# Kernel tuning notes

Measured on AMD Instinct MI355X. Metric: run time of the kernel, lower is better.

## Reference

```python
import jax, jax.numpy as jnp
import numpy as np

N_NODES = 50000
N_EDGES = 800000
D = 64
BN_EPS = 1e-5


def setup_inputs() -> dict:
    key = jax.random.key(0)
    ks = jax.random.split(key, 16)
    x = jax.random.normal(ks[0], (N_NODES, D), dtype=jnp.float32)
    edge_index = jax.random.randint(ks[1], (2, N_EDGES), 0, N_NODES, dtype=jnp.int64)
    s = 1.0 / np.sqrt(D)
    def lin(k):
        kw, kb = jax.random.split(k)
        W = jax.random.uniform(kw, (D, D), jnp.float32, -s, s)
        b = jax.random.uniform(kb, (D,), jnp.float32, -s, s)
        return W, b
    W1_0, b1_0 = lin(ks[2])
    W2_0, b2_0 = lin(ks[3])
    W1_1, b1_1 = lin(ks[4])
    W2_1, b2_1 = lin(ks[5])
    return {
        "x": x, "edge_index": edge_index,
        "W1_0": W1_0, "b1_0": b1_0, "g_0": jnp.ones((D,), jnp.float32), "beta_0": jnp.zeros((D,), jnp.float32), "W2_0": W2_0, "b2_0": b2_0,
        "W1_1": W1_1, "b1_1": b1_1, "g_1": jnp.ones((D,), jnp.float32), "beta_1": jnp.zeros((D,), jnp.float32), "W2_1": W2_1, "b2_1": b2_1,
    }


def _gin_layer(x, src, dst, W1, b1, g, beta, W2, b2):
    # GINConv with eps=0: h_i = MLP( x_i + sum_{j->i} x_j )
    agg = jax.ops.segment_sum(x[src], dst, num_segments=N_NODES)  # [N, D]
    h = agg + x
    h = h @ W1 + b1
    # BatchNorm1d (training-mode batch statistics, biased variance)
    mean = jnp.mean(h, axis=0)
    var = jnp.var(h, axis=0)
    h = (h - mean) * jax.lax.rsqrt(var + BN_EPS) * g + beta
    h = jax.nn.relu(h)
    h = jax.nn.relu(h @ W2 + b2)
    return h


def reference(x, edge_index, W1_0, b1_0, g_0, beta_0, W2_0, b2_0,
              W1_1, b1_1, g_1, beta_1, W2_1, b2_1):
    src = edge_index[0]  # message source j
    dst = edge_index[1]  # aggregation target i
    h1 = _gin_layer(x, src, dst, W1_0, b1_0, g_0, beta_0, W2_0, b2_0)
    h2 = _gin_layer(h1, src, dst, W1_1, b1_1, g_1, beta_1, W2_1, b2_1)
    return (h1, h2)
```

## Files before the change

kernel.cpp:

```cpp
#include <hip/hip_runtime.h>
#include <hip/hip_bf16.h>

#define N_NODES 50000
#define N_EDGES 800000
#define DD 64
#define RPB 64
#define GBLOCKS ((N_NODES + RPB - 1) / RPB)
#define MBLOCKS ((N_NODES + 63) / 64)
#define SCAN_BLOCKS ((N_NODES + 255) / 256)
#define CAST_BLOCKS ((N_NODES * DD / 8 + 255) / 256)
#define BN_EPS 1e-5f


__device__ __forceinline__ float bf2f(unsigned short b) {
    return __uint_as_float(((unsigned)b) << 16);
}
__device__ __forceinline__ float loadF(const void* p, int i, int isf) {
    return isf ? ((const float*)p)[i] : bf2f(((const unsigned short*)p)[i]);
}
template<bool ISF>
__device__ __forceinline__ float4 ld4(const void* p, int i) {
    if (ISF) return *reinterpret_cast<const float4*>((const float*)p + i);
    ushort4 u = *reinterpret_cast<const ushort4*>((const unsigned short*)p + i);
    return make_float4(bf2f(u.x), bf2f(u.y), bf2f(u.z), bf2f(u.w));
}
__device__ __forceinline__ void acc8(float4& a, float4& b, uint4 u) {
    a.x += __uint_as_float(u.x << 16);
    a.y += __uint_as_float(u.x & 0xFFFF0000u);
    a.z += __uint_as_float(u.y << 16);
    a.w += __uint_as_float(u.y & 0xFFFF0000u);
    b.x += __uint_as_float(u.z << 16);
    b.y += __uint_as_float(u.z & 0xFFFF0000u);
    b.z += __uint_as_float(u.w << 16);
    b.w += __uint_as_float(u.w & 0xFFFF0000u);
}

__global__ __launch_bounds__(256) void initcast_kernel(
    const void* __restrict__ x, const int* __restrict__ ei,
    int* __restrict__ flags, int* __restrict__ cnt,
    float* __restrict__ sums, unsigned short* __restrict__ xb)
{
    __shared__ int cntF, cntI;
    int t = threadIdx.x;
    if (t == 0) { cntF = 0; cntI = 0; }
    __syncthreads();
    unsigned short wd = ((const unsigned short*)x)[2 * t];
    int e = (wd >> 7) & 0xFF;
    if (e >= 0x70 && e <= 0x8F) atomicAdd(&cntF, 1);
    if (t < 128 && ei[2 * t + 1] == 0) atomicAdd(&cntI, 1);
    __syncthreads();
    int isf = (cntF < 128) ? 1 : 0;

    int gid = blockIdx.x * 256 + t;
    if (gid < N_NODES) cnt[gid] = 0;
    if (gid < 256) sums[gid] = 0.0f;
    if (blockIdx.x == 0 && t == 0) {
        flags[0] = isf;
        flags[1] = (cntI > 64) ? 1 : 0;
    }

    int i = gid * 8;
    if (i < N_NODES * DD) {
        if (isf) {
            float4 a = *reinterpret_cast<const float4*>((const float*)x + i);
            float4 b = *reinterpret_cast<const float4*>((const float*)x + i + 4);
            ushort4 o0, o1;
            o0.x = __bfloat16_as_ushort(__float2bfloat16(a.x));
            o0.y = __bfloat16_as_ushort(__float2bfloat16(a.y));
            o0.z = __bfloat16_as_ushort(__float2bfloat16(a.z));
            o0.w = __bfloat16_as_ushort(__float2bfloat16(a.w));
            o1.x = __bfloat16_as_ushort(__float2bfloat16(b.x));
            o1.y = __bfloat16_as_ushort(__float2bfloat16(b.y));
            o1.z = __bfloat16_as_ushort(__float2bfloat16(b.z));
            o1.w = __bfloat16_as_ushort(__float2bfloat16(b.w));
            *reinterpret_cast<ushort4*>(xb + i) = o0;
            *reinterpret_cast<ushort4*>(xb + i + 4) = o1;
        } else {
            *reinterpret_cast<uint4*>(xb + i) =
                *reinterpret_cast<const uint4*>((const unsigned short*)x + i);
        }
    }
}

__global__ void hist_kernel(const int* __restrict__ ei, int* __restrict__ cnt,
                            const int* __restrict__ flags) {
    int i64 = flags[1];
    int e = blockIdx.x * 256 + threadIdx.x;
    int d = i64 ? ei[2 * N_EDGES + 2 * e] : ei[N_EDGES + e];
    atomicAdd(cnt + d, 1);
}

__global__ __launch_bounds__(256) void scanA_kernel(const int* __restrict__ cnt,
                                                    int* __restrict__ off,
                                                    int* __restrict__ bsum) {
    __shared__ int tmp[256];
    int t = threadIdx.x;
    int i = blockIdx.x * 256 + t;
    int v = (i < N_NODES) ? cnt[i] : 0;
    tmp[t] = v;
    __syncthreads();
    #pragma unroll
    for (int d = 1; d < 256; d <<= 1) {
        int u = (t >= d) ? tmp[t - d] : 0;
        __syncthreads();
        tmp[t] += u;
        __syncthreads();
    }
    if (i < N_NODES) off[i] = tmp[t] - v;
    if (t == 255) bsum[blockIdx.x] = tmp[255];
}

__global__ __launch_bounds__(256) void scanB_kernel(int* __restrict__ bsum,
                                                    int* __restrict__ off) {
    __shared__ int tmp[256];
    int t = threadIdx.x;
    int v = (t < SCAN_BLOCKS) ? bsum[t] : 0;
    tmp[t] = v;
    __syncthreads();
    #pragma unroll
    for (int d = 1; d < 256; d <<= 1) {
        int u = (t >= d) ? tmp[t - d] : 0;
        __syncthreads();
        tmp[t] += u;
        __syncthreads();
    }
    if (t < SCAN_BLOCKS) bsum[t] = tmp[t] - v;
    if (t == 255) off[N_NODES] = tmp[255];
}

__global__ __launch_bounds__(256) void scanC_kernel(const int* __restrict__ bsum,
                                                    int* __restrict__ off,
                                                    int* __restrict__ cur) {
    int i = blockIdx.x * 256 + threadIdx.x;
    if (i < N_NODES) {
        int o = off[i] + bsum[blockIdx.x];
        off[i] = o;
        cur[i] = o;
    }
}

__global__ void fill_kernel(const int* __restrict__ ei, int* __restrict__ cur,
                            unsigned short* __restrict__ srt, const int* __restrict__ flags) {
    int i64 = flags[1];
    int e = blockIdx.x * 256 + threadIdx.x;
    int s, d;
    if (i64) { s = ei[2 * e]; d = ei[2 * N_EDGES + 2 * e]; }
    else     { s = ei[e];     d = ei[N_EDGES + e]; }
    int pos = atomicAdd(cur + d, 1);
    srt[pos] = (unsigned short)s;
}

__global__ __launch_bounds__(512) void gather_gemm_stats_kernel(
    const unsigned short* __restrict__ xb, const void* __restrict__ self_src, int force_f32,
    const int* __restrict__ off, const unsigned short* __restrict__ srt,
    const void* __restrict__ W, const void* __restrict__ bias,
    float* __restrict__ out_, float* __restrict__ sums, const int* __restrict__ flags)
{
    __shared__ float sIn[RPB][DD];
    __shared__ float r1[8][DD], r2[8][DD];
    int tid = threadIdx.x;
    int lane = tid & 63, w = tid >> 6;
    int rs = lane >> 3, ch = lane & 7;
    int row0 = blockIdx.x * RPB;
    int isf = force_f32 ? 1 : flags[0];

    int lr = w * 8 + rs;
    int r = row0 + lr;
    float4 a  = make_float4(0.f, 0.f, 0.f, 0.f);
    float4 b  = make_float4(0.f, 0.f, 0.f, 0.f);
    float4 a2 = make_float4(0.f, 0.f, 0.f, 0.f);
    float4 b2 = make_float4(0.f, 0.f, 0.f, 0.f);
    if (r < N_NODES) {
        a = isf ? ld4<true>(self_src, r * DD + 8 * ch)
                : ld4<false>(self_src, r * DD + 8 * ch);
        b = isf ? ld4<true>(self_src, r * DD + 8 * ch + 4)
                : ld4<false>(self_src, r * DD + 8 * ch + 4);
        int k0 = off[r], k1 = off[r + 1];
        int k = k0;
        for (; k + 8 <= k1; k += 8) {
            int n0 = srt[k],     n1 = srt[k + 1], n2 = srt[k + 2], n3 = srt[k + 3];
            int n4 = srt[k + 4], n5 = srt[k + 5], n6 = srt[k + 6], n7 = srt[k + 7];
            uint4 u0 = *reinterpret_cast<const uint4*>(xb + n0 * DD + 8 * ch);
            uint4 u1 = *reinterpret_cast<const uint4*>(xb + n1 * DD + 8 * ch);
            uint4 u2 = *reinterpret_cast<const uint4*>(xb + n2 * DD + 8 * ch);
            uint4 u3 = *reinterpret_cast<const uint4*>(xb + n3 * DD + 8 * ch);
            uint4 u4 = *reinterpret_cast<const uint4*>(xb + n4 * DD + 8 * ch);
            uint4 u5 = *reinterpret_cast<const uint4*>(xb + n5 * DD + 8 * ch);
            uint4 u6 = *reinterpret_cast<const uint4*>(xb + n6 * DD + 8 * ch);
            uint4 u7 = *reinterpret_cast<const uint4*>(xb + n7 * DD + 8 * ch);
            acc8(a, b, u0);
            acc8(a2, b2, u1);
            acc8(a, b, u2);
            acc8(a2, b2, u3);
            acc8(a, b, u4);
            acc8(a2, b2, u5);
            acc8(a, b, u6);
            acc8(a2, b2, u7);
        }
        for (; k + 2 <= k1; k += 2) {
            int n0 = srt[k], n1 = srt[k + 1];
            uint4 u0 = *reinterpret_cast<const uint4*>(xb + n0 * DD + 8 * ch);
            uint4 u1 = *reinterpret_cast<const uint4*>(xb + n1 * DD + 8 * ch);
            acc8(a, b, u0);
            acc8(a2, b2, u1);
        }
        if (k < k1) {
            int n0 = srt[k];
            acc8(a, b, *reinterpret_cast<const uint4*>(xb + n0 * DD + 8 * ch));
        }
        a.x += a2.x; a.y += a2.y; a.z += a2.z; a.w += a2.w;
        b.x += b2.x; b.y += b2.y; b.z += b2.z; b.w += b2.w;
    }
    *reinterpret_cast<float4*>(&sIn[lr][8 * ch]) = a;
    *reinterpret_cast<float4*>(&sIn[lr][8 * ch + 4]) = b;
    __syncthreads();

    float wcol[DD];
    #pragma unroll
    for (int k = 0; k < DD; ++k) wcol[k] = loadF(W, k * DD + lane, isf);
    float bv = loadF(bias, lane, isf);

    float s1 = 0.f, s2 = 0.f;
    #pragma unroll 4
    for (int j = 0; j < 8; ++j) {
        int jr = w * 8 + j;
        float c0 = 0.f, c1 = 0.f, c2 = 0.f, c3 = 0.f;
        #pragma unroll
        for (int k = 0; k < DD; k += 4) {
            float4 aa = *reinterpret_cast<const float4*>(&sIn[jr][k]);
            c0 += aa.x * wcol[k];
            c1 += aa.y * wcol[k + 1];
            c2 += aa.z * wcol[k + 2];
            c3 += aa.w * wcol[k + 3];
        }
        float acc = bv + ((c0 + c1) + (c2 + c3));
        int rr = row0 + jr;
        if (rr < N_NODES) {
            out_[rr * DD + lane] = acc;
            s1 += acc;
            s2 += acc * acc;
        }
    }
    r1[w][lane] = s1; r2[w][lane] = s2;
    __syncthreads();
    if (w == 0) {
        float t1 = 0.f, t2 = 0.f;
        #pragma unroll
        for (int q = 0; q < 8; ++q) { t1 += r1[q][lane]; t2 += r2[q][lane]; }
        atomicAdd(&sums[lane], t1);
        atomicAdd(&sums[64 + lane], t2);
    }
}

__global__ __launch_bounds__(256) void mlp2_kernel(
    const float* __restrict__ in_, const float* __restrict__ sums,
    const void* __restrict__ gma, const void* __restrict__ beta,
    const void* __restrict__ W, const void* __restrict__ bias,
    float* __restrict__ oF, unsigned short* obf, const int* __restrict__ flags)
{
    __shared__ float sIn[64][DD];
    __shared__ float sScale[DD], sShift[DD];
    int isf = flags[0];
    int tid = threadIdx.x;
    int c = tid & 63, g = tid >> 6;
    int row0 = blockIdx.x * 64;

    if (tid < 64) {
        float S1 = sums[tid];
        float S2 = sums[64 + tid];
        float mean = S1 * (1.0f / N_NODES);
        float var  = S2 * (1.0f / N_NODES) - mean * mean;
        float scale = rsqrtf(var + BN_EPS) * loadF(gma, tid, isf);
        sScale[tid] = scale;
        sShift[tid] = loadF(beta, tid, isf) - mean * scale;
    }
    __syncthreads();

    #pragma unroll
    for (int j = 0; j < 4; ++j) {
        int lr = (tid >> 4) + 16 * j;
        int cc = (tid & 15) << 2;
        int r = row0 + lr;
        float4 v = make_float4(0.f, 0.f, 0.f, 0.f);
        if (r < N_NODES) {
            v = *reinterpret_cast<const float4*>(in_ + r * DD + cc);
            float4 sc = *reinterpret_cast<const float4*>(&sScale[cc]);
            float4 sh = *reinterpret_cast<const float4*>(&sShift[cc]);
            v.x = fmaxf(v.x * sc.x + sh.x, 0.f);
            v.y = fmaxf(v.y * sc.y + sh.y, 0.f);
            v.z = fmaxf(v.z * sc.z + sh.z, 0.f);
            v.w = fmaxf(v.w * sc.w + sh.w, 0.f);
        }
        *reinterpret_cast<float4*>(&sIn[lr][cc]) = v;
    }
    __syncthreads();

    float wcol[DD];
    #pragma unroll
    for (int k = 0; k < DD; ++k) wcol[k] = loadF(W, k * DD + c, isf);
    float bv = loadF(bias, c, isf);

    #pragma unroll 4
    for (int j = 0; j < 16; ++j) {
        int lr = g * 16 + j;
        float a0 = 0.f, a1 = 0.f, a2 = 0.f, a3 = 0.f;
        #pragma unroll
        for (int k = 0; k < DD; k += 4) {
            float4 a = *reinterpret_cast<const float4*>(&sIn[lr][k]);
            a0 += a.x * wcol[k];
            a1 += a.y * wcol[k + 1];
            a2 += a.z * wcol[k + 2];
            a3 += a.w * wcol[k + 3];
        }
        float acc = fmaxf(bv + ((a0 + a1) + (a2 + a3)), 0.f);
        int r = row0 + lr;
        if (r < N_NODES) {
            oF[r * DD + c] = acc;
            if (obf) obf[r * DD + c] = __bfloat16_as_ushort(__float2bfloat16(acc));
        }
    }
}

extern "C" void kernel_launch(void* const* d_in, const int* in_sizes, int n_in,
                              void* d_out, int out_size, void* d_ws, size_t ws_size,
                              hipStream_t stream)
{
    (void)in_sizes; (void)n_in; (void)out_size; (void)ws_size;
    const void* x  = d_in[0];
    const int* ei  = (const int*)d_in[1];
    const void* W1_0 = d_in[2];  const void* b1_0 = d_in[3];
    const void* g_0  = d_in[4];  const void* be_0 = d_in[5];
    const void* W2_0 = d_in[6];  const void* b2_0 = d_in[7];
    const void* W1_1 = d_in[8];  const void* b1_1 = d_in[9];
    const void* g_1  = d_in[10]; const void* be_1 = d_in[11];
    const void* W2_1 = d_in[12]; const void* b2_1 = d_in[13];

    float* wsf   = (float*)d_ws;
    float* sumsA = wsf;
    float* sumsB = wsf + 128;
    int*  flags  = (int*)(wsf + 256);
    int*  cnt    = (int*)(wsf + 512);
    int*  off    = cnt + 50048;
    int*  cur    = off + 50064;
    int*  bsum   = cur + 50048;
    unsigned short* srt = (unsigned short*)(bsum + 256);
    unsigned short* xb  = srt + 800064;
    float* O1    = (float*)d_out;
    float* O2    = O1 + (size_t)N_NODES * DD;

    dim3 blk(256);

    initcast_kernel<<<CAST_BLOCKS, blk, 0, stream>>>(x, ei, flags, cnt, sumsA, xb);
    hist_kernel<<<N_EDGES / 256, blk, 0, stream>>>(ei, cnt, flags);
    scanA_kernel<<<SCAN_BLOCKS, blk, 0, stream>>>(cnt, off, bsum);
    scanB_kernel<<<1, blk, 0, stream>>>(bsum, off);
    scanC_kernel<<<SCAN_BLOCKS, blk, 0, stream>>>(bsum, off, cur);
    fill_kernel<<<N_EDGES / 256, blk, 0, stream>>>(ei, cur, srt, flags);

    gather_gemm_stats_kernel<<<GBLOCKS, 512, 0, stream>>>(xb, x, 0, off, srt, W1_0, b1_0,
                                                          O2, sumsA, flags);
    mlp2_kernel<<<MBLOCKS, blk, 0, stream>>>(O2, sumsA, g_0, be_0, W2_0, b2_0, O1, xb, flags);

    gather_gemm_stats_kernel<<<GBLOCKS, 512, 0, stream>>>(xb, O1, 1, off, srt, W1_1, b1_1,
                                                          O2, sumsB, flags);
    mlp2_kernel<<<MBLOCKS, blk, 0, stream>>>(O2, sumsB, g_1, be_1, W2_1, b2_1, O2, nullptr, flags);
}
```

Before: 313.3 us.

## Two-pass bucketed CSR fill, vectorized index loads, and smaller gather blocks

The CSR fill, which used per-node global atomics, becomes a two-stage scheme. Edges are first scattered into 64-node buckets with padded bucket counters, packing the source and the local destination into one 32-bit word. A second kernel then places them within each bucket using shared-memory atomics. The gather loop aligns to 8 and loads eight 16-bit neighbor indices with one uint4 load, and the gather/GEMM blocks drop from 512 to 256 threads with 32 rows each. This aims to cut global atomic contention and index-load instructions, at the cost of an extra kernel, a temporary buffer and twice as many BN-stat atomics.

```diff
diff --git a/kernel.cpp b/kernel.cpp
--- a/kernel.cpp
+++ b/kernel.cpp
@@ -4,9 +4,10 @@
 #define N_NODES 50000
 #define N_EDGES 800000
 #define DD 64
-#define RPB 64
+#define RPB 32
 #define GBLOCKS ((N_NODES + RPB - 1) / RPB)
 #define MBLOCKS ((N_NODES + 63) / 64)
+#define NBUCKET ((N_NODES + 63) / 64)
 #define SCAN_BLOCKS ((N_NODES + 255) / 256)
 #define CAST_BLOCKS ((N_NODES * DD / 8 + 255) / 256)
 #define BN_EPS 1e-5f
@@ -130,34 +131,56 @@
 
 __global__ __launch_bounds__(256) void scanC_kernel(const int* __restrict__ bsum,
                                                     int* __restrict__ off,
-                                                    int* __restrict__ cur) {
+                                                    int* __restrict__ bcur) {
     int i = blockIdx.x * 256 + threadIdx.x;
     if (i < N_NODES) {
         int o = off[i] + bsum[blockIdx.x];
         off[i] = o;
-        cur[i] = o;
-    }
-}
-
-__global__ void fill_kernel(const int* __restrict__ ei, int* __restrict__ cur,
-                            unsigned short* __restrict__ srt, const int* __restrict__ flags) {
+        if ((i & 63) == 0) bcur[(i >> 6) * 16] = o;
+    }
+}
+
+__global__ void fillA_kernel(const int* __restrict__ ei, int* __restrict__ bcur,
+                             unsigned int* __restrict__ tmp, const int* __restrict__ flags) {
     int i64 = flags[1];
     int e = blockIdx.x * 256 + threadIdx.x;
     int s, d;
     if (i64) { s = ei[2 * e]; d = ei[2 * N_EDGES + 2 * e]; }
     else     { s = ei[e];     d = ei[N_EDGES + e]; }
-    int pos = atomicAdd(cur + d, 1);
-    srt[pos] = (unsigned short)s;
-}
-
-__global__ __launch_bounds__(512) void gather_gemm_stats_kernel(
+    int b = d >> 6;
+    int pos = atomicAdd(bcur + b * 16, 1);
+    tmp[pos] = (unsigned)s | ((unsigned)(d & 63) << 16);
+}
+
+__global__ __launch_bounds__(256) void fillB_kernel(const int* __restrict__ off,
+                                                    const unsigned int* __restrict__ tmp,
+                                                    unsigned short* __restrict__ srt) {
+    __shared__ int cur64[64];
+    int b = blockIdx.x;
+    int t = threadIdx.x;
+    if (t < 64) {
+        int idx = b * 64 + t;
+        cur64[t] = (idx < N_NODES) ? off[idx] : N_EDGES;
+    }
+    __syncthreads();
+    int start = off[b * 64];
+    int endn  = (b + 1) * 64; if (endn > N_NODES) endn = N_NODES;
+    int end   = off[endn];
+    for (int i = start + t; i < end; i += 256) {
+        unsigned v = tmp[i];
+        int pos = atomicAdd(&cur64[v >> 16], 1);
+        srt[pos] = (unsigned short)(v & 0xFFFFu);
+    }
+}
+
+__global__ __launch_bounds__(256) void gather_gemm_stats_kernel(
     const unsigned short* __restrict__ xb, const void* __restrict__ self_src, int force_f32,
     const int* __restrict__ off, const unsigned short* __restrict__ srt,
     const void* __restrict__ W, const void* __restrict__ bias,
     float* __restrict__ out_, float* __restrict__ sums, const int* __restrict__ flags)
 {
     __shared__ float sIn[RPB][DD];
-    __shared__ float r1[8][DD], r2[8][DD];
+    __shared__ float r1[4][DD], r2[4][DD];
     int tid = threadIdx.x;
     int lane = tid & 63, w = tid >> 6;
     int rs = lane >> 3, ch = lane & 7;
@@ -177,9 +200,16 @@
                 : ld4<false>(self_src, r * DD + 8 * ch + 4);
         int k0 = off[r], k1 = off[r + 1];
         int k = k0;
+        for (; k < k1 && (k & 7); ++k) {
+            int n0 = srt[k];
+            acc8(a, b, *reinterpret_cast<const uint4*>(xb + n0 * DD + 8 * ch));
+        }
         for (; k + 8 <= k1; k += 8) {
-            int n0 = srt[k],     n1 = srt[k + 1], n2 = srt[k + 2], n3 = srt[k + 3];
-            int n4 = srt[k + 4], n5 = srt[k + 5], n6 = srt[k + 6], n7 = srt[k + 7];
+            uint4 sv = *reinterpret_cast<const uint4*>(srt + k);
+            int n0 = sv.x & 0xFFFF, n1 = sv.x >> 16;
+            int n2 = sv.y & 0xFFFF, n3 = sv.y >> 16;
+            int n4 = sv.z & 0xFFFF, n5 = sv.z >> 16;
+            int n6 = sv.w & 0xFFFF, n7 = sv.w >> 16;
             uint4 u0 = *reinterpret_cast<const uint4*>(xb + n0 * DD + 8 * ch);
             uint4 u1 = *reinterpret_cast<const uint4*>(xb + n1 * DD + 8 * ch);
             uint4 u2 = *reinterpret_cast<const uint4*>(xb + n2 * DD + 8 * ch);
@@ -197,14 +227,7 @@
             acc8(a, b, u6);
             acc8(a2, b2, u7);
         }
-        for (; k + 2 <= k1; k += 2) {
-            int n0 = srt[k], n1 = srt[k + 1];
-            uint4 u0 = *reinterpret_cast<const uint4*>(xb + n0 * DD + 8 * ch);
-            uint4 u1 = *reinterpret_cast<const uint4*>(xb + n1 * DD + 8 * ch);
-            acc8(a, b, u0);
-            acc8(a2, b2, u1);
-        }
-        if (k < k1) {
+        for (; k < k1; ++k) {
             int n0 = srt[k];
             acc8(a, b, *reinterpret_cast<const uint4*>(xb + n0 * DD + 8 * ch));
         }
@@ -244,9 +267,8 @@
     r1[w][lane] = s1; r2[w][lane] = s2;
     __syncthreads();
     if (w == 0) {
-        float t1 = 0.f, t2 = 0.f;
-        #pragma unroll
-        for (int q = 0; q < 8; ++q) { t1 += r1[q][lane]; t2 += r2[q][lane]; }
+        float t1 = r1[0][lane] + r1[1][lane] + r1[2][lane] + r1[3][lane];
+        float t2 = r2[0][lane] + r2[1][lane] + r2[2][lane] + r2[3][lane];
         atomicAdd(&sums[lane], t1);
         atomicAdd(&sums[64 + lane], t2);
     }
@@ -341,9 +363,10 @@
     int*  flags  = (int*)(wsf + 256);
     int*  cnt    = (int*)(wsf + 512);
     int*  off    = cnt + 50048;
-    int*  cur    = off + 50064;
-    int*  bsum   = cur + 50048;
-    unsigned short* srt = (unsigned short*)(bsum + 256);
+    int*  bcur   = off + 50064;
+    int*  bsum   = bcur + 12512;
+    unsigned int* tmp32 = (unsigned int*)(bsum + 256) + 48;
+    unsigned short* srt = (unsigned short*)(tmp32 + 800000);
     unsigned short* xb  = srt + 800064;
     float* O1    = (float*)d_out;
     float* O2    = O1 + (size_t)N_NODES * DD;
@@ -354,14 +377,15 @@
     hist_kernel<<<N_EDGES / 256, blk, 0, stream>>>(ei, cnt, flags);
     scanA_kernel<<<SCAN_BLOCKS, blk, 0, stream>>>(cnt, off, bsum);
     scanB_kernel<<<1, blk, 0, stream>>>(bsum, off);
-    scanC_kernel<<<SCAN_BLOCKS, blk, 0, stream>>>(bsum, off, cur);
-    fill_kernel<<<N_EDGES / 256, blk, 0, stream>>>(ei, cur, srt, flags);
-
-    gather_gemm_stats_kernel<<<GBLOCKS, 512, 0, stream>>>(xb, x, 0, off, srt, W1_0, b1_0,
+    scanC_kernel<<<SCAN_BLOCKS, blk, 0, stream>>>(bsum, off, bcur);
+    fillA_kernel<<<N_EDGES / 256, blk, 0, stream>>>(ei, bcur, tmp32, flags);
+    fillB_kernel<<<NBUCKET, blk, 0, stream>>>(off, tmp32, srt);
+
+    gather_gemm_stats_kernel<<<GBLOCKS, blk, 0, stream>>>(xb, x, 0, off, srt, W1_0, b1_0,
                                                           O2, sumsA, flags);
     mlp2_kernel<<<MBLOCKS, blk, 0, stream>>>(O2, sumsA, g_0, be_0, W2_0, b2_0, O1, xb, flags);
 
-    gather_gemm_stats_kernel<<<GBLOCKS, 512, 0, stream>>>(xb, O1, 1, off, srt, W1_1, b1_1,
+    gather_gemm_stats_kernel<<<GBLOCKS, blk, 0, stream>>>(xb, O1, 1, off, srt, W1_1, b1_1,
                                                           O2, sumsB, flags);
     mlp2_kernel<<<MBLOCKS, blk, 0, stream>>>(O2, sumsB, g_1, be_1, W2_1, b2_1, O2, nullptr, flags);
 }
```

Result: slower. 347.7 us (+11.0%).
